# Kernel optimization log

Hardware: AMD Instinct MI355X
Metric: run time of the kernel (lower is better)

The kernel has to match this reference:

```python
import jax, jax.numpy as jnp
import numpy as np

EPS = 0.01       # perturbation radius (constructor arg)
MEAN = 0.1307    # MNIST normalize constants from the 'else' branch
SIGMA = 0.3081


def _get_bound(v, eps):
    # torch get_bound detaches eps before taking |.| and summing
    r = jnp.sum(jnp.abs(jax.lax.stop_gradient(eps)), axis=-1)
    return v + r, v - r


def _relu_zono(v, eps):
    # v: [N], eps: [N, E]. Append one fresh (zero) error column, as the torch code does.
    n = v.shape[0]
    eps = jnp.concatenate([eps, jnp.zeros((n, 1), eps.dtype)], axis=-1)  # [N, E+1]
    u, l = _get_bound(v, eps)
    denom = u - l  # = 2*sum|eps| >= 0; guard against 0 for non-crossing rows
    # slopes are created as Parameters = u/(u-l) on the first pass (detached leaf)
    slope = jax.lax.stop_gradient(u / jnp.where(denom == 0, 1.0, denom))
    # at init slope == base = u/(u-l), so the slope <= base branch is taken
    term = (1.0 - slope) * u * 0.5
    crossing = (u > 0) & (l < 0)
    dead = u <= 0
    # torch uses slope.data * values.data for the linear part, + term (term carries grad)
    v_cross = jax.lax.stop_gradient(slope * v) + term
    v_new = jnp.where(dead, 0.0, jnp.where(crossing, v_cross, v))
    eps_cross = jnp.concatenate([slope[:, None] * eps[:, :-1], term[:, None]], axis=-1)
    eps_new = jnp.where(dead[:, None], 0.0, jnp.where(crossing[:, None], eps_cross, eps))
    return v_new, eps_new


def _forward(inputs, W1, b1, W2, b2, W3, b3):
    # initial zonotope build (faithful to source: values = u + l, radii = values - l = u)
    upper = jnp.minimum(inputs + EPS, 1.0)   # upper - relu(upper - 1)
    lower = jnp.maximum(inputs - EPS, 0.0)   # relu(lower)
    values = upper + lower
    eps = jnp.diag((values - lower).flatten())  # [D, D]
    # Normalize layer (the 'else' branch)
    values = (values - MEAN) / SIGMA
    eps = eps / SIGMA
    # Flatten
    v = values.flatten()
    # Linear -> ReLU -> Linear -> ReLU -> Linear
    v = W1 @ v + b1
    eps = W1 @ eps
    v, eps = _relu_zono(v, eps)
    v = W2 @ v + b2
    eps = W2 @ eps
    v, eps = _relu_zono(v, eps)
    v = W3 @ v + b3
    eps = W3 @ eps
    u, l = _get_bound(v, eps)
    return u, l


def setup_inputs() -> dict:
    key = jax.random.key(0)
    ks = jax.random.split(key, 7)
    D, H, O = 1024, 4096, 10
    inputs = jax.random.uniform(ks[0], (1, 1, 32, 32), jnp.float32)
    W1 = jax.random.normal(ks[1], (H, D), jnp.float32) / np.float32(np.sqrt(D))
    b1 = jax.random.normal(ks[2], (H,), jnp.float32) * 0.01
    W2 = jax.random.normal(ks[3], (H, H), jnp.float32) / np.float32(np.sqrt(H))
    b2 = jax.random.normal(ks[4], (H,), jnp.float32) * 0.01
    W3 = jax.random.normal(ks[5], (O, H), jnp.float32) / np.float32(np.sqrt(H))
    b3 = jax.random.normal(ks[6], (O,), jnp.float32) * 0.01
    return {"inputs": inputs, "W1": W1, "b1": b1, "W2": W2, "b2": b2, "W3": W3, "b3": b3}


def reference(inputs, W1, b1, W2, b2, W3, b3):
    return _forward(inputs, W1, b1, W2, b2, W3, b3)
```

## Files before the change

kernel.cpp:

```cpp
#include <hip/hip_runtime.h>
#include <math.h>

#define ZEPS  0.01f
#define ZMEAN 0.1307f
#define ZSIGMA 0.3081f

constexpr int D = 1024, H = 4096, O = 10;

using short8 = __attribute__((ext_vector_type(8))) short;
using f32x4  = __attribute__((ext_vector_type(4))) float;
typedef unsigned short ushort_t;

__device__ inline unsigned short f2bf(float x) {
    unsigned int u = __float_as_uint(x);
    u += 0x7FFFu + ((u >> 16) & 1u);
    return (unsigned short)(u >> 16);
}
__device__ inline float bf2f(unsigned short h) {
    return __uint_as_float(((unsigned int)h) << 16);
}
__device__ inline unsigned int f2bf2(float a, float b) {
    return (unsigned int)f2bf(a) | ((unsigned int)f2bf(b) << 16);
}

__device__ inline void gl_lds16(const void* g, void* l) {
    __builtin_amdgcn_global_load_lds(
        (const __attribute__((address_space(1))) unsigned int*)g,
        (__attribute__((address_space(3))) unsigned int*)l, 16, 0, 0);
}

__device__ inline float zval(float xv) {
    float up = fminf(xv + ZEPS, 1.f);
    float lo = fmaxf(xv - ZEPS, 0.f);
    return (up + lo - ZMEAN) / ZSIGMA;
}
__device__ inline float zdia(float xv) {
    return fminf(xv + ZEPS, 1.f) / ZSIGMA;
}

__device__ inline void relu_params(float v, float r, float& vout, float& aout, float& tout) {
    float u = v + r, l = v - r;
    float denom = u - l;
    float slope = u / (denom == 0.f ? 1.f : denom);
    float term = (1.f - slope) * u * 0.5f;
    bool dead = (u <= 0.f);
    bool crossing = (u > 0.f) && (l < 0.f);
    vout = dead ? 0.f : (crossing ? (slope * v + term) : v);
    aout = dead ? 0.f : (crossing ? slope : 1.f);
    tout = (!dead && crossing) ? term : 0.f;
}

__global__ __launch_bounds__(256) void k_pre(const float* __restrict__ W1, const float* __restrict__ b1,
                                             const float* __restrict__ x,
                                             float* __restrict__ v1p, float* __restrict__ a1,
                                             float* __restrict__ t1,
                                             const float* __restrict__ W2, ushort_t* __restrict__ W2bf,
                                             float* __restrict__ pbufR) {
    int b = blockIdx.x;
    if (b < 2048) {
        const float* src = W2 + (size_t)b * 8192;
        ushort_t* dst = W2bf + (size_t)b * 8192;
#pragma unroll
        for (int it = 0; it < 4; ++it) {
            int j = it * 2048 + threadIdx.x * 8;
            float4 w0 = *(const float4*)&src[j];
            float4 w1 = *(const float4*)&src[j + 4];
            uint4 o;
            o.x = f2bf2(w0.x, w0.y);
            o.y = f2bf2(w0.z, w0.w);
            o.z = f2bf2(w1.x, w1.y);
            o.w = f2bf2(w1.z, w1.w);
            *(uint4*)&dst[j] = o;
        }
    } else if (b < 3072) {
        int wid = threadIdx.x >> 6, lane = threadIdx.x & 63;
        int i = (b - 2048) * 4 + wid;
        const float* row = W1 + (size_t)i * D;
        float sv = 0.f, sr = 0.f;
#pragma unroll
        for (int it = 0; it < 4; ++it) {
            int j = it * 256 + lane * 4;
            float4 w = *(const float4*)&row[j];
            float4 xx = *(const float4*)&x[j];
            sv += w.x * zval(xx.x) + w.y * zval(xx.y) + w.z * zval(xx.z) + w.w * zval(xx.w);
            sr += fabsf(w.x) * zdia(xx.x) + fabsf(w.y) * zdia(xx.y) +
                  fabsf(w.z) * zdia(xx.z) + fabsf(w.w) * zdia(xx.w);
        }
#pragma unroll
        for (int m = 1; m <= 32; m <<= 1) {
            sv += __shfl_xor(sv, m, 64);
            sr += __shfl_xor(sr, m, 64);
        }
        if (lane == 0) {
            float vo, ao, to;
            relu_params(sv + b1[i], sr, vo, ao, to);
            v1p[i] = vo; a1[i] = ao; t1[i] = to;
        }
    } else {
        for (int k = threadIdx.x; k < O * D; k += 256) pbufR[k] = 0.f;
    }
}

__global__ __launch_bounds__(256) void k_mid(const float* __restrict__ W1, const float* __restrict__ a1,
                                             const float* __restrict__ x, ushort_t* __restrict__ W1sT,
                                             const float* __restrict__ W2, const float* __restrict__ v1p,
                                             const float* __restrict__ t1,
                                             float* __restrict__ v2raw, float* __restrict__ t2raw) {
    int b = blockIdx.x;
    if (b < 1024) {
        int wid = threadIdx.x >> 6, lane = threadIdx.x & 63;
        int i = b * 4 + wid;
        const float* row = W2 + (size_t)i * H;
        float sv = 0.f, st = 0.f;
#pragma unroll 2
        for (int it = 0; it < 8; ++it) {
            int j = it * 512 + lane * 8;
            float4 w0 = *(const float4*)&row[j];
            float4 w1 = *(const float4*)&row[j + 4];
            float4 v0 = *(const float4*)&v1p[j];
            float4 v1 = *(const float4*)&v1p[j + 4];
            float4 t0 = *(const float4*)&t1[j];
            float4 t1v = *(const float4*)&t1[j + 4];
            sv += w0.x * v0.x + w0.y * v0.y + w0.z * v0.z + w0.w * v0.w
                + w1.x * v1.x + w1.y * v1.y + w1.z * v1.z + w1.w * v1.w;
            st += w0.x * t0.x + w0.y * t0.y + w0.z * t0.z + w0.w * t0.w
                + w1.x * t1v.x + w1.y * t1v.y + w1.z * t1v.z + w1.w * t1v.w;
        }
#pragma unroll
        for (int m = 1; m <= 32; m <<= 1) {
            sv += __shfl_xor(sv, m, 64);
            st += __shfl_xor(st, m, 64);
        }
        if (lane == 0) { v2raw[i] = sv; t2raw[i] = st; }
    } else {
        __shared__ float tile[32][33];
        int bb = b - 1024;
        int j0 = (bb & 31) * 32, k0 = (bb >> 5) * 32;
        int r = threadIdx.x >> 3;
        int c = (threadIdx.x & 7) * 4;
        float4 w = *(const float4*)&W1[(size_t)(k0 + r) * D + j0 + c];
        float4 xx = *(const float4*)&x[j0 + c];
        float a = a1[k0 + r];
        tile[r][c + 0] = a * w.x * zdia(xx.x);
        tile[r][c + 1] = a * w.y * zdia(xx.y);
        tile[r][c + 2] = a * w.z * zdia(xx.z);
        tile[r][c + 3] = a * w.w * zdia(xx.w);
        __syncthreads();
        ushort4 o;
        o.x = f2bf(tile[c + 0][r]);
        o.y = f2bf(tile[c + 1][r]);
        o.z = f2bf(tile[c + 2][r]);
        o.w = f2bf(tile[c + 3][r]);
        *(ushort4*)&W1sT[(size_t)(j0 + r) * H + k0 + c] = o;
    }
}

#define GBK 64
__global__ __launch_bounds__(256) void k_gemm_mfma(const ushort_t* __restrict__ A,
                                                   const ushort_t* __restrict__ B,
                                                   ushort_t* __restrict__ C) {
    const int N = D, K = H;
    __shared__ __align__(16) ushort_t As[2][128 * GBK];
    __shared__ __align__(16) ushort_t Bs[2][128 * GBK];
    int orig = blockIdx.x;
    int b = (orig & 7) * 64 + (orig >> 3);
    int z  = b >> 8;
    int xn = (b >> 5) & 7;
    int ym = b & 31;
    int tid = threadIdx.x;
    int wave = tid >> 6, lane = tid & 63;
    int bm = ym * 128, bn = xn * 128;
    int kbeg = z * (K / 2);
    ushort_t* Cz = C + (size_t)z * ((size_t)H * D);
    int wm = (wave >> 1) * 64, wn = (wave & 1) * 64;

    int srow = lane >> 3, scp = (lane & 7) ^ srow;
    int r15 = lane & 15, quad = lane >> 4, key = r15 & 7;

    const int S = (K / 2) / GBK;

    const ushort_t* Ab = A + (size_t)(bm + wave * 32 + srow) * K + kbeg + scp * 8;
    const ushort_t* Bb = B + (size_t)(bn + wave * 32 + srow) * K + kbeg + scp * 8;

    auto issue = [&](int t, int buf) {
#pragma unroll
        for (int g = 0; g < 4; ++g)
            gl_lds16(Ab + (size_t)(g * 8) * K + t * GBK, &As[buf][(wave * 32 + g * 8) * GBK]);
#pragma unroll
        for (int g = 0; g < 4; ++g)
            gl_lds16(Bb + (size_t)(g * 8) * K + t * GBK, &Bs[buf][(wave * 32 + g * 8) * GBK]);
    };

    f32x4 acc[4][4];
#pragma unroll
    for (int p = 0; p < 4; ++p)
#pragma unroll
        for (int q = 0; q < 4; ++q) acc[p][q] = (f32x4){0.f, 0.f, 0.f, 0.f};

    issue(0, 0);
    __syncthreads();

    for (int t = 0; t < S; ++t) {
        int buf = t & 1, nbuf = buf ^ 1;
        if (t + 1 < S) issue(t + 1, nbuf);
#pragma unroll
        for (int kk = 0; kk < 2; ++kk) {
            short8 af[4], bfr[4];
#pragma unroll
            for (int mt = 0; mt < 4; ++mt)
                af[mt] = *(const short8*)&As[buf][(wm + mt * 16 + r15) * GBK + (((kk * 4 + quad) ^ key)) * 8];
#pragma unroll
            for (int nt = 0; nt < 4; ++nt)
                bfr[nt] = *(const short8*)&Bs[buf][(wn + nt * 16 + r15) * GBK + (((kk * 4 + quad) ^ key)) * 8];
#pragma unroll
            for (int mt = 0; mt < 4; ++mt)
#pragma unroll
                for (int nt = 0; nt < 4; ++nt)
                    acc[mt][nt] = __builtin_amdgcn_mfma_f32_16x16x32_bf16(af[mt], bfr[nt], acc[mt][nt], 0, 0, 0);
        }
        __syncthreads();
    }

#pragma unroll
    for (int mt = 0; mt < 4; ++mt) {
        int gr = bm + wm + mt * 16 + quad * 4;
#pragma unroll
        for (int nt = 0; nt < 4; ++nt) {
            int gc = bn + wn + nt * 16 + r15;
            Cz[(size_t)(gr + 0) * N + gc] = f2bf(acc[mt][nt][0]);
            Cz[(size_t)(gr + 1) * N + gc] = f2bf(acc[mt][nt][1]);
            Cz[(size_t)(gr + 2) * N + gc] = f2bf(acc[mt][nt][2]);
            Cz[(size_t)(gr + 3) * N + gc] = f2bf(acc[mt][nt][3]);
        }
    }
}

__global__ __launch_bounds__(256) void k_relu2(const ushort_t* __restrict__ e1, const ushort_t* __restrict__ e2,
                                               const float* __restrict__ v2raw, const float* __restrict__ t2raw,
                                               const float* __restrict__ b2, const float* __restrict__ W3,
                                               float* __restrict__ v2p, float* __restrict__ a2,
                                               float* __restrict__ t2, float* __restrict__ t2col,
                                               float* __restrict__ w3s) {
    int wid = threadIdx.x >> 6, lane = threadIdx.x & 63;
    int i = blockIdx.x * 4 + wid;
    float s = 0.f;
#pragma unroll
    for (int it = 0; it < 2; ++it) {
        int j = lane * 8 + it * 512;
        ushort4 a0 = *(const ushort4*)&e1[(size_t)i * D + j];
        ushort4 a1v = *(const ushort4*)&e1[(size_t)i * D + j + 4];
        ushort4 b0 = *(const ushort4*)&e2[(size_t)i * D + j];
        ushort4 b1v = *(const ushort4*)&e2[(size_t)i * D + j + 4];
        s += fabsf(bf2f(a0.x) + bf2f(b0.x)) + fabsf(bf2f(a0.y) + bf2f(b0.y))
           + fabsf(bf2f(a0.z) + bf2f(b0.z)) + fabsf(bf2f(a0.w) + bf2f(b0.w))
           + fabsf(bf2f(a1v.x) + bf2f(b1v.x)) + fabsf(bf2f(a1v.y) + bf2f(b1v.y))
           + fabsf(bf2f(a1v.z) + bf2f(b1v.z)) + fabsf(bf2f(a1v.w) + bf2f(b1v.w));
    }
#pragma unroll
    for (int m = 1; m <= 32; m <<= 1) s += __shfl_xor(s, m, 64);
    float ve = v2raw[i];
    float te = t2raw[i];
    float vo, ao, to;
    relu_params(ve + b2[i], s + fabsf(te), vo, ao, to);
    if (lane == 0) { v2p[i] = vo; a2[i] = ao; t2[i] = to; t2col[i] = te; }
    if (lane < O) w3s[(size_t)i * O + lane] = W3[(size_t)lane * H + i] * ao;
}

__global__ __launch_bounds__(256) void k_eps3a(const ushort_t* __restrict__ e1, const ushort_t* __restrict__ e2,
                                               const float* __restrict__ w3s,
                                               float* __restrict__ pbufR) {
    int jb = blockIdx.x, ib = blockIdx.y;
    int jj = threadIdx.x & 15, s = threadIdx.x >> 4;
    int j = jb * 64 + jj * 4;
    int i0 = ib * 128 + s * 8;
    float acc[4][O];
#pragma unroll
    for (int c = 0; c < 4; ++c)
#pragma unroll
        for (int o = 0; o < O; ++o) acc[c][o] = 0.f;
    for (int ii = 0; ii < 8; ++ii) {
        int i = i0 + ii;
        ushort4 a = *(const ushort4*)&e1[(size_t)i * D + j];
        ushort4 b = *(const ushort4*)&e2[(size_t)i * D + j];
        float e0 = bf2f(a.x) + bf2f(b.x), ee1 = bf2f(a.y) + bf2f(b.y);
        float ee2 = bf2f(a.z) + bf2f(b.z), ee3 = bf2f(a.w) + bf2f(b.w);
        const float* w = &w3s[(size_t)i * O];
#pragma unroll
        for (int o = 0; o < O; ++o) {
            float wo = w[o];
            acc[0][o] += wo * e0; acc[1][o] += wo * ee1;
            acc[2][o] += wo * ee2; acc[3][o] += wo * ee3;
        }
    }
    __shared__ float sm[16][64][O];
#pragma unroll
    for (int c = 0; c < 4; ++c)
#pragma unroll
        for (int o = 0; o < O; ++o) sm[s][jj * 4 + c][o] = acc[c][o];
    __syncthreads();
    for (int idx = threadIdx.x; idx < 64 * O; idx += 256) {
        int col = idx / O, o = idx % O;
        float t = 0.f;
#pragma unroll
        for (int ss = 0; ss < 16; ++ss) t += sm[ss][col][o];
        atomicAdd(&pbufR[(size_t)o * D + jb * 64 + col], t);
    }
}

__global__ __launch_bounds__(256) void k_final(const float* __restrict__ W3, const float* __restrict__ b3,
                                               const float* __restrict__ v2p, const float* __restrict__ a2,
                                               const float* __restrict__ t2col, const float* __restrict__ t2,
                                               const float* __restrict__ pbufR, float* __restrict__ out) {
    int o = blockIdx.x, tid = threadIdx.x;
    float s3 = 0.f;
    for (int j = tid; j < D; j += 256) s3 += fabsf(pbufR[(size_t)o * D + j]);
    const float* row = W3 + (size_t)o * H;
    float sv = 0.f, s1 = 0.f, s2 = 0.f;
    for (int i = tid; i < H; i += 256) {
        float w = row[i];
        sv += w * v2p[i];
        s1 += w * a2[i] * t2col[i];
        s2 += w * t2[i];
    }
    __shared__ float ra[256], rb[256], rc[256], rd[256];
    ra[tid] = sv; rb[tid] = s1; rc[tid] = s2; rd[tid] = s3;
    __syncthreads();
    for (int off = 128; off; off >>= 1) {
        if (tid < off) {
            ra[tid] += ra[tid + off]; rb[tid] += rb[tid + off];
            rc[tid] += rc[tid + off]; rd[tid] += rd[tid + off];
        }
        __syncthreads();
    }
    if (tid == 0) {
        float v3 = ra[0] + b3[o];
        float rr = rd[0] + fabsf(rb[0]) + fabsf(rc[0]);
        out[o] = v3 + rr;
        out[O + o] = v3 - rr;
    }
}

extern "C" void kernel_launch(void* const* d_in, const int* in_sizes, int n_in,
                              void* d_out, int out_size, void* d_ws, size_t ws_size,
                              hipStream_t stream) {
    const float* x  = (const float*)d_in[0];
    const float* W1 = (const float*)d_in[1];
    const float* b1 = (const float*)d_in[2];
    const float* W2 = (const float*)d_in[3];
    const float* b2 = (const float*)d_in[4];
    const float* W3 = (const float*)d_in[5];
    const float* b3 = (const float*)d_in[6];
    float* out = (float*)d_out;

    float* p = (float*)d_ws;
    float* v1p    = p; p += H;
    float* a1     = p; p += H;
    float* t1     = p; p += H;
    float* t2col  = p; p += H;
    float* v2p    = p; p += H;
    float* a2     = p; p += H;
    float* t2     = p; p += H;
    float* v2raw  = p; p += H;
    float* t2raw  = p; p += H;
    float* w3s    = p; p += H * O + 8;
    float* pbufR  = p; p += O * D + 8;
    ushort_t* eps2  = (ushort_t*)p;
    ushort_t* W1sT  = eps2 + (size_t)2 * H * D;
    ushort_t* W2bf  = W1sT + (size_t)H * D;
    ushort_t* eps2b = eps2 + (size_t)H * D;

    k_pre<<<3073, 256, 0, stream>>>(W1, b1, x, v1p, a1, t1, W2, W2bf, pbufR);
    k_mid<<<5120, 256, 0, stream>>>(W1, a1, x, W1sT, W2, v1p, t1, v2raw, t2raw);
    k_gemm_mfma<<<512, 256, 0, stream>>>(W2bf, W1sT, eps2);
    k_relu2<<<H / 4, 256, 0, stream>>>(eps2, eps2b, v2raw, t2raw, b2, W3, v2p, a2, t2, t2col, w3s);
    k_eps3a<<<dim3(D / 64, 32), 256, 0, stream>>>(eps2, eps2b, w3s, pbufR);
    k_final<<<O, 256, 0, stream>>>(W3, b3, v2p, a2, t2col, t2, pbufR, out);
}
```

Before: 223.5 us.

## Fuse W2 bf16 conversion into matvec, drop split-K GEMM, fold relu2 into epilogue

The W2 fp32-to-bf16 conversion moves into the k_mid matvec so W2 is read from memory once instead of twice. The GEMM stops splitting K into two halves and uses 128x64 tiles over the full K, so only one bf16 eps matrix is written and no second partial has to be summed. The GEMM epilogue accumulates per-row |eps| sums into r2acc with atomics, which removes the separate k_relu2 pass over eps. The relu parameters are recomputed inside k_eps3a and k_final. The trade-off is a longer K loop per block with a smaller N tile, plus atomic traffic in the epilogue.

```diff
diff --git a/kernel.cpp b/kernel.cpp
--- a/kernel.cpp
+++ b/kernel.cpp
@@ -54,27 +54,11 @@
                                              const float* __restrict__ x,
                                              float* __restrict__ v1p, float* __restrict__ a1,
                                              float* __restrict__ t1,
-                                             const float* __restrict__ W2, ushort_t* __restrict__ W2bf,
-                                             float* __restrict__ pbufR) {
+                                             float* __restrict__ r2acc, float* __restrict__ pbufR) {
     int b = blockIdx.x;
-    if (b < 2048) {
-        const float* src = W2 + (size_t)b * 8192;
-        ushort_t* dst = W2bf + (size_t)b * 8192;
-#pragma unroll
-        for (int it = 0; it < 4; ++it) {
-            int j = it * 2048 + threadIdx.x * 8;
-            float4 w0 = *(const float4*)&src[j];
-            float4 w1 = *(const float4*)&src[j + 4];
-            uint4 o;
-            o.x = f2bf2(w0.x, w0.y);
-            o.y = f2bf2(w0.z, w0.w);
-            o.z = f2bf2(w1.x, w1.y);
-            o.w = f2bf2(w1.z, w1.w);
-            *(uint4*)&dst[j] = o;
-        }
-    } else if (b < 3072) {
+    if (b < 1024) {
         int wid = threadIdx.x >> 6, lane = threadIdx.x & 63;
-        int i = (b - 2048) * 4 + wid;
+        int i = b * 4 + wid;
         const float* row = W1 + (size_t)i * D;
         float sv = 0.f, sr = 0.f;
 #pragma unroll
@@ -97,6 +81,7 @@
             v1p[i] = vo; a1[i] = ao; t1[i] = to;
         }
     } else {
+        for (int k = threadIdx.x; k < H; k += 256) r2acc[k] = 0.f;
         for (int k = threadIdx.x; k < O * D; k += 256) pbufR[k] = 0.f;
     }
 }
@@ -104,13 +89,14 @@
 __global__ __launch_bounds__(256) void k_mid(const float* __restrict__ W1, const float* __restrict__ a1,
                                              const float* __restrict__ x, ushort_t* __restrict__ W1sT,
                                              const float* __restrict__ W2, const float* __restrict__ v1p,
-                                             const float* __restrict__ t1,
+                                             const float* __restrict__ t1, ushort_t* __restrict__ W2bf,
                                              float* __restrict__ v2raw, float* __restrict__ t2raw) {
     int b = blockIdx.x;
     if (b < 1024) {
         int wid = threadIdx.x >> 6, lane = threadIdx.x & 63;
         int i = b * 4 + wid;
         const float* row = W2 + (size_t)i * H;
+        ushort_t* orow = W2bf + (size_t)i * H;
         float sv = 0.f, st = 0.f;
 #pragma unroll 2
         for (int it = 0; it < 8; ++it) {
@@ -125,6 +111,12 @@
                 + w1.x * v1.x + w1.y * v1.y + w1.z * v1.z + w1.w * v1.w;
             st += w0.x * t0.x + w0.y * t0.y + w0.z * t0.z + w0.w * t0.w
                 + w1.x * t1v.x + w1.y * t1v.y + w1.z * t1v.z + w1.w * t1v.w;
+            uint4 o;
+            o.x = f2bf2(w0.x, w0.y);
+            o.y = f2bf2(w0.z, w0.w);
+            o.z = f2bf2(w1.x, w1.y);
+            o.w = f2bf2(w1.z, w1.w);
+            *(uint4*)&orow[j] = o;
         }
 #pragma unroll
         for (int m = 1; m <= 32; m <<= 1) {
@@ -158,44 +150,42 @@
 #define GBK 64
 __global__ __launch_bounds__(256) void k_gemm_mfma(const ushort_t* __restrict__ A,
                                                    const ushort_t* __restrict__ B,
-                                                   ushort_t* __restrict__ C) {
+                                                   ushort_t* __restrict__ C,
+                                                   float* __restrict__ r2acc) {
     const int N = D, K = H;
     __shared__ __align__(16) ushort_t As[2][128 * GBK];
-    __shared__ __align__(16) ushort_t Bs[2][128 * GBK];
+    __shared__ __align__(16) ushort_t Bs[2][64 * GBK];
     int orig = blockIdx.x;
     int b = (orig & 7) * 64 + (orig >> 3);
-    int z  = b >> 8;
-    int xn = (b >> 5) & 7;
-    int ym = b & 31;
+    int ym = b >> 4;
+    int xn = b & 15;
     int tid = threadIdx.x;
     int wave = tid >> 6, lane = tid & 63;
-    int bm = ym * 128, bn = xn * 128;
-    int kbeg = z * (K / 2);
-    ushort_t* Cz = C + (size_t)z * ((size_t)H * D);
-    int wm = (wave >> 1) * 64, wn = (wave & 1) * 64;
+    int bm = ym * 128, bn = xn * 64;
+    int wm = (wave >> 1) * 64, wn = (wave & 1) * 32;
 
     int srow = lane >> 3, scp = (lane & 7) ^ srow;
     int r15 = lane & 15, quad = lane >> 4, key = r15 & 7;
 
-    const int S = (K / 2) / GBK;
-
-    const ushort_t* Ab = A + (size_t)(bm + wave * 32 + srow) * K + kbeg + scp * 8;
-    const ushort_t* Bb = B + (size_t)(bn + wave * 32 + srow) * K + kbeg + scp * 8;
+    const int S = K / GBK;
+
+    const ushort_t* Ab = A + (size_t)(bm + wave * 32 + srow) * K + scp * 8;
+    const ushort_t* Bb = B + (size_t)(bn + wave * 16 + srow) * K + scp * 8;
 
     auto issue = [&](int t, int buf) {
 #pragma unroll
         for (int g = 0; g < 4; ++g)
             gl_lds16(Ab + (size_t)(g * 8) * K + t * GBK, &As[buf][(wave * 32 + g * 8) * GBK]);
 #pragma unroll
-        for (int g = 0; g < 4; ++g)
-            gl_lds16(Bb + (size_t)(g * 8) * K + t * GBK, &Bs[buf][(wave * 32 + g * 8) * GBK]);
+        for (int g = 0; g < 2; ++g)
+            gl_lds16(Bb + (size_t)(g * 8) * K + t * GBK, &Bs[buf][(wave * 16 + g * 8) * GBK]);
     };
 
-    f32x4 acc[4][4];
+    f32x4 acc[4][2];
 #pragma unroll
     for (int p = 0; p < 4; ++p)
 #pragma unroll
-        for (int q = 0; q < 4; ++q) acc[p][q] = (f32x4){0.f, 0.f, 0.f, 0.f};
+        for (int q = 0; q < 2; ++q) acc[p][q] = (f32x4){0.f, 0.f, 0.f, 0.f};
 
     issue(0, 0);
     __syncthreads();
@@ -205,74 +195,79 @@
         if (t + 1 < S) issue(t + 1, nbuf);
 #pragma unroll
         for (int kk = 0; kk < 2; ++kk) {
-            short8 af[4], bfr[4];
+            short8 af[4], bfr[2];
 #pragma unroll
             for (int mt = 0; mt < 4; ++mt)
                 af[mt] = *(const short8*)&As[buf][(wm + mt * 16 + r15) * GBK + (((kk * 4 + quad) ^ key)) * 8];
 #pragma unroll
-            for (int nt = 0; nt < 4; ++nt)
+            for (int nt = 0; nt < 2; ++nt)
                 bfr[nt] = *(const short8*)&Bs[buf][(wn + nt * 16 + r15) * GBK + (((kk * 4 + quad) ^ key)) * 8];
 #pragma unroll
             for (int mt = 0; mt < 4; ++mt)
 #pragma unroll
-                for (int nt = 0; nt < 4; ++nt)
+                for (int nt = 0; nt < 2; ++nt)
                     acc[mt][nt] = __builtin_amdgcn_mfma_f32_16x16x32_bf16(af[mt], bfr[nt], acc[mt][nt], 0, 0, 0);
         }
         __syncthreads();
     }
 
+    float rsum[4][4];
+#pragma unroll
+    for (int mt = 0; mt < 4; ++mt)
+#pragma unroll
+        for (int rg = 0; rg < 4; ++rg) rsum[mt][rg] = 0.f;
 #pragma unroll
     for (int mt = 0; mt < 4; ++mt) {
         int gr = bm + wm + mt * 16 + quad * 4;
 #pragma unroll
-        for (int nt = 0; nt < 4; ++nt) {
+        for (int nt = 0; nt < 2; ++nt) {
             int gc = bn + wn + nt * 16 + r15;
-            Cz[(size_t)(gr + 0) * N + gc] = f2bf(acc[mt][nt][0]);
-            Cz[(size_t)(gr + 1) * N + gc] = f2bf(acc[mt][nt][1]);
-            Cz[(size_t)(gr + 2) * N + gc] = f2bf(acc[mt][nt][2]);
-            Cz[(size_t)(gr + 3) * N + gc] = f2bf(acc[mt][nt][3]);
-        }
-    }
-}
-
-__global__ __launch_bounds__(256) void k_relu2(const ushort_t* __restrict__ e1, const ushort_t* __restrict__ e2,
-                                               const float* __restrict__ v2raw, const float* __restrict__ t2raw,
-                                               const float* __restrict__ b2, const float* __restrict__ W3,
-                                               float* __restrict__ v2p, float* __restrict__ a2,
-                                               float* __restrict__ t2, float* __restrict__ t2col,
-                                               float* __restrict__ w3s) {
-    int wid = threadIdx.x >> 6, lane = threadIdx.x & 63;
-    int i = blockIdx.x * 4 + wid;
-    float s = 0.f;
-#pragma unroll
-    for (int it = 0; it < 2; ++it) {
-        int j = lane * 8 + it * 512;
-        ushort4 a0 = *(const ushort4*)&e1[(size_t)i * D + j];
-        ushort4 a1v = *(const ushort4*)&e1[(size_t)i * D + j + 4];
-        ushort4 b0 = *(const ushort4*)&e2[(size_t)i * D + j];
-        ushort4 b1v = *(const ushort4*)&e2[(size_t)i * D + j + 4];
-        s += fabsf(bf2f(a0.x) + bf2f(b0.x)) + fabsf(bf2f(a0.y) + bf2f(b0.y))
-           + fabsf(bf2f(a0.z) + bf2f(b0.z)) + fabsf(bf2f(a0.w) + bf2f(b0.w))
-           + fabsf(bf2f(a1v.x) + bf2f(b1v.x)) + fabsf(bf2f(a1v.y) + bf2f(b1v.y))
-           + fabsf(bf2f(a1v.z) + bf2f(b1v.z)) + fabsf(bf2f(a1v.w) + bf2f(b1v.w));
-    }
-#pragma unroll
-    for (int m = 1; m <= 32; m <<= 1) s += __shfl_xor(s, m, 64);
-    float ve = v2raw[i];
-    float te = t2raw[i];
-    float vo, ao, to;
-    relu_params(ve + b2[i], s + fabsf(te), vo, ao, to);
-    if (lane == 0) { v2p[i] = vo; a2[i] = ao; t2[i] = to; t2col[i] = te; }
-    if (lane < O) w3s[(size_t)i * O + lane] = W3[(size_t)lane * H + i] * ao;
-}
-
-__global__ __launch_bounds__(256) void k_eps3a(const ushort_t* __restrict__ e1, const ushort_t* __restrict__ e2,
-                                               const float* __restrict__ w3s,
+            f32x4 a = acc[mt][nt];
+#pragma unroll
+            for (int rg = 0; rg < 4; ++rg) {
+                ushort_t hb = f2bf(a[rg]);
+                C[(size_t)(gr + rg) * N + gc] = hb;
+                rsum[mt][rg] += fabsf(bf2f(hb));
+            }
+        }
+    }
+#pragma unroll
+    for (int mt = 0; mt < 4; ++mt)
+#pragma unroll
+        for (int rg = 0; rg < 4; ++rg) {
+            float v = rsum[mt][rg];
+            v += __shfl_xor(v, 1, 64);
+            v += __shfl_xor(v, 2, 64);
+            v += __shfl_xor(v, 4, 64);
+            v += __shfl_xor(v, 8, 64);
+            if (r15 == 0)
+                atomicAdd(&r2acc[bm + wm + mt * 16 + quad * 4 + rg], v);
+        }
+}
+
+__global__ __launch_bounds__(256) void k_eps3a(const ushort_t* __restrict__ e,
+                                               const float* __restrict__ r2acc,
+                                               const float* __restrict__ v2raw,
+                                               const float* __restrict__ t2raw,
+                                               const float* __restrict__ b2,
+                                               const float* __restrict__ W3,
                                                float* __restrict__ pbufR) {
     int jb = blockIdx.x, ib = blockIdx.y;
+    __shared__ float w3sm[128][O];
+    int i0b = ib * 128;
+    if (threadIdx.x < 128) {
+        int i = i0b + threadIdx.x;
+        float te = t2raw[i];
+        float vo, ao, to;
+        relu_params(v2raw[i] + b2[i], r2acc[i] + fabsf(te), vo, ao, to);
+#pragma unroll
+        for (int o = 0; o < O; ++o) w3sm[threadIdx.x][o] = W3[(size_t)o * H + i] * ao;
+    }
+    __syncthreads();
+
     int jj = threadIdx.x & 15, s = threadIdx.x >> 4;
     int j = jb * 64 + jj * 4;
-    int i0 = ib * 128 + s * 8;
+    int i0 = i0b + s * 8;
     float acc[4][O];
 #pragma unroll
     for (int c = 0; c < 4; ++c)
@@ -280,11 +275,10 @@
         for (int o = 0; o < O; ++o) acc[c][o] = 0.f;
     for (int ii = 0; ii < 8; ++ii) {
         int i = i0 + ii;
-        ushort4 a = *(const ushort4*)&e1[(size_t)i * D + j];
-        ushort4 b = *(const ushort4*)&e2[(size_t)i * D + j];
-        float e0 = bf2f(a.x) + bf2f(b.x), ee1 = bf2f(a.y) + bf2f(b.y);
-        float ee2 = bf2f(a.z) + bf2f(b.z), ee3 = bf2f(a.w) + bf2f(b.w);
-        const float* w = &w3s[(size_t)i * O];
+        ushort4 a = *(const ushort4*)&e[(size_t)i * D + j];
+        float e0 = bf2f(a.x), ee1 = bf2f(a.y);
+        float ee2 = bf2f(a.z), ee3 = bf2f(a.w);
+        const float* w = &w3sm[i - i0b][0];
 #pragma unroll
         for (int o = 0; o < O; ++o) {
             float wo = w[o];
@@ -308,8 +302,10 @@
 }
 
 __global__ __launch_bounds__(256) void k_final(const float* __restrict__ W3, const float* __restrict__ b3,
-                                               const float* __restrict__ v2p, const float* __restrict__ a2,
-                                               const float* __restrict__ t2col, const float* __restrict__ t2,
+                                               const float* __restrict__ r2acc,
+                                               const float* __restrict__ v2raw,
+                                               const float* __restrict__ t2raw,
+                                               const float* __restrict__ b2,
                                                const float* __restrict__ pbufR, float* __restrict__ out) {
     int o = blockIdx.x, tid = threadIdx.x;
     float s3 = 0.f;
@@ -318,9 +314,12 @@
     float sv = 0.f, s1 = 0.f, s2 = 0.f;
     for (int i = tid; i < H; i += 256) {
         float w = row[i];
-        sv += w * v2p[i];
-        s1 += w * a2[i] * t2col[i];
-        s2 += w * t2[i];
+        float te = t2raw[i];
+        float vo, ao, to;
+        relu_params(v2raw[i] + b2[i], r2acc[i] + fabsf(te), vo, ao, to);
+        sv += w * vo;
+        s1 += w * ao * te;
+        s2 += w * to;
     }
     __shared__ float ra[256], rb[256], rc[256], rd[256];
     ra[tid] = sv; rb[tid] = s1; rc[tid] = s2; rd[tid] = s3;
@@ -356,23 +355,17 @@
     float* v1p    = p; p += H;
     float* a1     = p; p += H;
     float* t1     = p; p += H;
-    float* t2col  = p; p += H;
-    float* v2p    = p; p += H;
-    float* a2     = p; p += H;
-    float* t2     = p; p += H;
     float* v2raw  = p; p += H;
     float* t2raw  = p; p += H;
-    float* w3s    = p; p += H * O + 8;
+    float* r2acc  = p; p += H;
     float* pbufR  = p; p += O * D + 8;
-    ushort_t* eps2  = (ushort_t*)p;
-    ushort_t* W1sT  = eps2 + (size_t)2 * H * D;
+    ushort_t* eps   = (ushort_t*)p;
+    ushort_t* W1sT  = eps + (size_t)H * D;
     ushort_t* W2bf  = W1sT + (size_t)H * D;
-    ushort_t* eps2b = eps2 + (size_t)H * D;
-
-    k_pre<<<3073, 256, 0, stream>>>(W1, b1, x, v1p, a1, t1, W2, W2bf, pbufR);
-    k_mid<<<5120, 256, 0, stream>>>(W1, a1, x, W1sT, W2, v1p, t1, v2raw, t2raw);
-    k_gemm_mfma<<<512, 256, 0, stream>>>(W2bf, W1sT, eps2);
-    k_relu2<<<H / 4, 256, 0, stream>>>(eps2, eps2b, v2raw, t2raw, b2, W3, v2p, a2, t2, t2col, w3s);
-    k_eps3a<<<dim3(D / 64, 32), 256, 0, stream>>>(eps2, eps2b, w3s, pbufR);
-    k_final<<<O, 256, 0, stream>>>(W3, b3, v2p, a2, t2col, t2, pbufR, out);
-}
+
+    k_pre<<<1025, 256, 0, stream>>>(W1, b1, x, v1p, a1, t1, r2acc, pbufR);
+    k_mid<<<5120, 256, 0, stream>>>(W1, a1, x, W1sT, W2, v1p, t1, W2bf, v2raw, t2raw);
+    k_gemm_mfma<<<512, 256, 0, stream>>>(W2bf, W1sT, eps, r2acc);
+    k_eps3a<<<dim3(D / 64, 32), 256, 0, stream>>>(eps, r2acc, v2raw, t2raw, b2, W3, pbufR);
+    k_final<<<O, 256, 0, stream>>>(W3, b3, r2acc, v2raw, t2raw, b2, pbufR, out);
+}
```

Result: slower. 245.3 us (+9.8%).

## Fuse W2 bf16 conversion into matvec and merge relu2 with eps3 reduction

Applied to the files above, without the earlier changes.

The W2 fp32-to-bf16 conversion moves from k_pre into the k_mid matvec loop, so W2 is read from global memory once instead of twice. k_relu2 and k_eps3a are merged into one k_epsfuse kernel: each block computes the ReLU parameters for 16 rows, keeps the scaled W3 slice in LDS, and accumulates those rows' eps contributions. The atomic accumulation now targets 32 partitioned partial buffers, and k_final sums them. The GEMM block-index mapping also changes from the swizzled order to a plain one, which may alter L2 locality. The trade-offs are more atomics per thread and only 256 blocks in the fused kernel.

```diff
diff --git a/kernel.cpp b/kernel.cpp
--- a/kernel.cpp
+++ b/kernel.cpp
@@ -8,6 +8,7 @@
 constexpr int D = 1024, H = 4096, O = 10;
 
 using short8 = __attribute__((ext_vector_type(8))) short;
+using us8    = __attribute__((ext_vector_type(8))) unsigned short;
 using f32x4  = __attribute__((ext_vector_type(4))) float;
 typedef unsigned short ushort_t;
 
@@ -54,27 +55,11 @@
                                              const float* __restrict__ x,
                                              float* __restrict__ v1p, float* __restrict__ a1,
                                              float* __restrict__ t1,
-                                             const float* __restrict__ W2, ushort_t* __restrict__ W2bf,
-                                             float* __restrict__ pbufR) {
+                                             float* __restrict__ pbufP) {
     int b = blockIdx.x;
-    if (b < 2048) {
-        const float* src = W2 + (size_t)b * 8192;
-        ushort_t* dst = W2bf + (size_t)b * 8192;
-#pragma unroll
-        for (int it = 0; it < 4; ++it) {
-            int j = it * 2048 + threadIdx.x * 8;
-            float4 w0 = *(const float4*)&src[j];
-            float4 w1 = *(const float4*)&src[j + 4];
-            uint4 o;
-            o.x = f2bf2(w0.x, w0.y);
-            o.y = f2bf2(w0.z, w0.w);
-            o.z = f2bf2(w1.x, w1.y);
-            o.w = f2bf2(w1.z, w1.w);
-            *(uint4*)&dst[j] = o;
-        }
-    } else if (b < 3072) {
+    if (b < 1024) {
         int wid = threadIdx.x >> 6, lane = threadIdx.x & 63;
-        int i = (b - 2048) * 4 + wid;
+        int i = b * 4 + wid;
         const float* row = W1 + (size_t)i * D;
         float sv = 0.f, sr = 0.f;
 #pragma unroll
@@ -97,20 +82,23 @@
             v1p[i] = vo; a1[i] = ao; t1[i] = to;
         }
     } else {
-        for (int k = threadIdx.x; k < O * D; k += 256) pbufR[k] = 0.f;
+        int zb = b - 1024;
+        size_t base = (size_t)zb * 5120;
+        for (int k = threadIdx.x; k < 5120; k += 256) pbufP[base + k] = 0.f;
     }
 }
 
 __global__ __launch_bounds__(256) void k_mid(const float* __restrict__ W1, const float* __restrict__ a1,
                                              const float* __restrict__ x, ushort_t* __restrict__ W1sT,
                                              const float* __restrict__ W2, const float* __restrict__ v1p,
-                                             const float* __restrict__ t1,
+                                             const float* __restrict__ t1, ushort_t* __restrict__ W2bf,
                                              float* __restrict__ v2raw, float* __restrict__ t2raw) {
     int b = blockIdx.x;
     if (b < 1024) {
         int wid = threadIdx.x >> 6, lane = threadIdx.x & 63;
         int i = b * 4 + wid;
         const float* row = W2 + (size_t)i * H;
+        ushort_t* orow = W2bf + (size_t)i * H;
         float sv = 0.f, st = 0.f;
 #pragma unroll 2
         for (int it = 0; it < 8; ++it) {
@@ -125,6 +113,12 @@
                 + w1.x * v1.x + w1.y * v1.y + w1.z * v1.z + w1.w * v1.w;
             st += w0.x * t0.x + w0.y * t0.y + w0.z * t0.z + w0.w * t0.w
                 + w1.x * t1v.x + w1.y * t1v.y + w1.z * t1v.z + w1.w * t1v.w;
+            uint4 o;
+            o.x = f2bf2(w0.x, w0.y);
+            o.y = f2bf2(w0.z, w0.w);
+            o.z = f2bf2(w1.x, w1.y);
+            o.w = f2bf2(w1.z, w1.w);
+            *(uint4*)&orow[j] = o;
         }
 #pragma unroll
         for (int m = 1; m <= 32; m <<= 1) {
@@ -162,33 +156,32 @@
     const int N = D, K = H;
     __shared__ __align__(16) ushort_t As[2][128 * GBK];
     __shared__ __align__(16) ushort_t Bs[2][128 * GBK];
-    int orig = blockIdx.x;
-    int b = (orig & 7) * 64 + (orig >> 3);
-    int z  = b >> 8;
-    int xn = (b >> 5) & 7;
-    int ym = b & 31;
+    int b = blockIdx.x;
+    int xb = b & 7;
+    int v = b >> 3;
+    int z = v & 1;
+    int y = v >> 1;
     int tid = threadIdx.x;
     int wave = tid >> 6, lane = tid & 63;
-    int bm = ym * 128, bn = xn * 128;
+    int bm = y * 128, bn = xb * 128;
     int kbeg = z * (K / 2);
     ushort_t* Cz = C + (size_t)z * ((size_t)H * D);
     int wm = (wave >> 1) * 64, wn = (wave & 1) * 64;
 
-    int srow = lane >> 3, scp = (lane & 7) ^ srow;
+    int srow = lane >> 3, sc = lane & 7, scp = sc ^ srow;
     int r15 = lane & 15, quad = lane >> 4, key = r15 & 7;
 
     const int S = (K / 2) / GBK;
 
-    const ushort_t* Ab = A + (size_t)(bm + wave * 32 + srow) * K + kbeg + scp * 8;
-    const ushort_t* Bb = B + (size_t)(bn + wave * 32 + srow) * K + kbeg + scp * 8;
-
-    auto issue = [&](int t, int buf) {
-#pragma unroll
-        for (int g = 0; g < 4; ++g)
-            gl_lds16(Ab + (size_t)(g * 8) * K + t * GBK, &As[buf][(wave * 32 + g * 8) * GBK]);
-#pragma unroll
-        for (int g = 0; g < 4; ++g)
-            gl_lds16(Bb + (size_t)(g * 8) * K + t * GBK, &Bs[buf][(wave * 32 + g * 8) * GBK]);
+    auto issue = [&](int s, int buf) {
+#pragma unroll
+        for (int g = 0; g < 4; ++g) {
+            int row = wave * 32 + g * 8;
+            gl_lds16(&A[(size_t)(bm + row + srow) * K + kbeg + s * GBK + scp * 8],
+                     &As[buf][row * GBK]);
+            gl_lds16(&B[(size_t)(bn + row + srow) * K + kbeg + s * GBK + scp * 8],
+                     &Bs[buf][row * GBK]);
+        }
     };
 
     f32x4 acc[4][4];
@@ -200,9 +193,9 @@
     issue(0, 0);
     __syncthreads();
 
-    for (int t = 0; t < S; ++t) {
-        int buf = t & 1, nbuf = buf ^ 1;
-        if (t + 1 < S) issue(t + 1, nbuf);
+    for (int s = 0; s < S; ++s) {
+        int buf = s & 1, nbuf = buf ^ 1;
+        if (s + 1 < S) issue(s + 1, nbuf);
 #pragma unroll
         for (int kk = 0; kk < 2; ++kk) {
             short8 af[4], bfr[4];
@@ -235,91 +228,87 @@
     }
 }
 
-__global__ __launch_bounds__(256) void k_relu2(const ushort_t* __restrict__ e1, const ushort_t* __restrict__ e2,
-                                               const float* __restrict__ v2raw, const float* __restrict__ t2raw,
-                                               const float* __restrict__ b2, const float* __restrict__ W3,
-                                               float* __restrict__ v2p, float* __restrict__ a2,
-                                               float* __restrict__ t2, float* __restrict__ t2col,
-                                               float* __restrict__ w3s) {
-    int wid = threadIdx.x >> 6, lane = threadIdx.x & 63;
-    int i = blockIdx.x * 4 + wid;
-    float s = 0.f;
-#pragma unroll
-    for (int it = 0; it < 2; ++it) {
-        int j = lane * 8 + it * 512;
-        ushort4 a0 = *(const ushort4*)&e1[(size_t)i * D + j];
-        ushort4 a1v = *(const ushort4*)&e1[(size_t)i * D + j + 4];
-        ushort4 b0 = *(const ushort4*)&e2[(size_t)i * D + j];
-        ushort4 b1v = *(const ushort4*)&e2[(size_t)i * D + j + 4];
-        s += fabsf(bf2f(a0.x) + bf2f(b0.x)) + fabsf(bf2f(a0.y) + bf2f(b0.y))
-           + fabsf(bf2f(a0.z) + bf2f(b0.z)) + fabsf(bf2f(a0.w) + bf2f(b0.w))
-           + fabsf(bf2f(a1v.x) + bf2f(b1v.x)) + fabsf(bf2f(a1v.y) + bf2f(b1v.y))
-           + fabsf(bf2f(a1v.z) + bf2f(b1v.z)) + fabsf(bf2f(a1v.w) + bf2f(b1v.w));
-    }
-#pragma unroll
-    for (int m = 1; m <= 32; m <<= 1) s += __shfl_xor(s, m, 64);
-    float ve = v2raw[i];
-    float te = t2raw[i];
-    float vo, ao, to;
-    relu_params(ve + b2[i], s + fabsf(te), vo, ao, to);
-    if (lane == 0) { v2p[i] = vo; a2[i] = ao; t2[i] = to; t2col[i] = te; }
-    if (lane < O) w3s[(size_t)i * O + lane] = W3[(size_t)lane * H + i] * ao;
-}
-
-__global__ __launch_bounds__(256) void k_eps3a(const ushort_t* __restrict__ e1, const ushort_t* __restrict__ e2,
-                                               const float* __restrict__ w3s,
-                                               float* __restrict__ pbufR) {
-    int jb = blockIdx.x, ib = blockIdx.y;
-    int jj = threadIdx.x & 15, s = threadIdx.x >> 4;
-    int j = jb * 64 + jj * 4;
-    int i0 = ib * 128 + s * 8;
+__global__ __launch_bounds__(256) void k_epsfuse(const ushort_t* __restrict__ e1, const ushort_t* __restrict__ e2,
+                                                 const float* __restrict__ v2raw, const float* __restrict__ t2raw,
+                                                 const float* __restrict__ b2, const float* __restrict__ W3,
+                                                 float* __restrict__ v2p, float* __restrict__ a2,
+                                                 float* __restrict__ t2, float* __restrict__ pbufP) {
+    __shared__ float w3sm[16][O];
+    int b = blockIdx.x, tid = threadIdx.x;
+    int wid = tid >> 6, lane = tid & 63;
+    int i0 = b * 16;
+
+#pragma unroll
+    for (int rr = 0; rr < 4; ++rr) {
+        int il = wid * 4 + rr;
+        int i = i0 + il;
+        const ushort_t* p1 = &e1[(size_t)i * D + lane * 16];
+        const ushort_t* p2 = &e2[(size_t)i * D + lane * 16];
+        float s = 0.f;
+#pragma unroll
+        for (int q = 0; q < 2; ++q) {
+            us8 u1 = *(const us8*)(p1 + q * 8);
+            us8 u2 = *(const us8*)(p2 + q * 8);
+#pragma unroll
+            for (int e = 0; e < 8; ++e) s += fabsf(bf2f(u1[e]) + bf2f(u2[e]));
+        }
+#pragma unroll
+        for (int m = 1; m <= 32; m <<= 1) s += __shfl_xor(s, m, 64);
+        float te = t2raw[i];
+        float vo, ao, to;
+        relu_params(v2raw[i] + b2[i], s + fabsf(te), vo, ao, to);
+        if (lane == 0) { v2p[i] = vo; a2[i] = ao; t2[i] = to; }
+        if (lane < O) w3sm[il][lane] = W3[(size_t)lane * H + i] * ao;
+    }
+    __syncthreads();
+
+    int j = tid * 4;
     float acc[4][O];
 #pragma unroll
     for (int c = 0; c < 4; ++c)
 #pragma unroll
         for (int o = 0; o < O; ++o) acc[c][o] = 0.f;
-    for (int ii = 0; ii < 8; ++ii) {
-        int i = i0 + ii;
+#pragma unroll 4
+    for (int il = 0; il < 16; ++il) {
+        int i = i0 + il;
         ushort4 a = *(const ushort4*)&e1[(size_t)i * D + j];
-        ushort4 b = *(const ushort4*)&e2[(size_t)i * D + j];
-        float e0 = bf2f(a.x) + bf2f(b.x), ee1 = bf2f(a.y) + bf2f(b.y);
-        float ee2 = bf2f(a.z) + bf2f(b.z), ee3 = bf2f(a.w) + bf2f(b.w);
-        const float* w = &w3s[(size_t)i * O];
+        ushort4 bb = *(const ushort4*)&e2[(size_t)i * D + j];
+        float es0 = bf2f(a.x) + bf2f(bb.x), es1 = bf2f(a.y) + bf2f(bb.y);
+        float es2 = bf2f(a.z) + bf2f(bb.z), es3 = bf2f(a.w) + bf2f(bb.w);
+        const float* w = &w3sm[il][0];
 #pragma unroll
         for (int o = 0; o < O; ++o) {
             float wo = w[o];
-            acc[0][o] += wo * e0; acc[1][o] += wo * ee1;
-            acc[2][o] += wo * ee2; acc[3][o] += wo * ee3;
-        }
-    }
-    __shared__ float sm[16][64][O];
-#pragma unroll
-    for (int c = 0; c < 4; ++c)
-#pragma unroll
-        for (int o = 0; o < O; ++o) sm[s][jj * 4 + c][o] = acc[c][o];
-    __syncthreads();
-    for (int idx = threadIdx.x; idx < 64 * O; idx += 256) {
-        int col = idx / O, o = idx % O;
-        float t = 0.f;
-#pragma unroll
-        for (int ss = 0; ss < 16; ++ss) t += sm[ss][col][o];
-        atomicAdd(&pbufR[(size_t)o * D + jb * 64 + col], t);
-    }
+            acc[0][o] += wo * es0; acc[1][o] += wo * es1;
+            acc[2][o] += wo * es2; acc[3][o] += wo * es3;
+        }
+    }
+    float* pg = &pbufP[(size_t)(b & 31) * O * D];
+#pragma unroll
+    for (int o = 0; o < O; ++o)
+#pragma unroll
+        for (int c = 0; c < 4; ++c)
+            atomicAdd(&pg[(size_t)o * D + j + c], acc[c][o]);
 }
 
 __global__ __launch_bounds__(256) void k_final(const float* __restrict__ W3, const float* __restrict__ b3,
                                                const float* __restrict__ v2p, const float* __restrict__ a2,
-                                               const float* __restrict__ t2col, const float* __restrict__ t2,
-                                               const float* __restrict__ pbufR, float* __restrict__ out) {
+                                               const float* __restrict__ t2, const float* __restrict__ t2raw,
+                                               const float* __restrict__ pbufP, float* __restrict__ out) {
     int o = blockIdx.x, tid = threadIdx.x;
     float s3 = 0.f;
-    for (int j = tid; j < D; j += 256) s3 += fabsf(pbufR[(size_t)o * D + j]);
+    for (int j = tid; j < D; j += 256) {
+        float t = 0.f;
+#pragma unroll
+        for (int g = 0; g < 32; ++g) t += pbufP[((size_t)g * O + o) * D + j];
+        s3 += fabsf(t);
+    }
     const float* row = W3 + (size_t)o * H;
     float sv = 0.f, s1 = 0.f, s2 = 0.f;
     for (int i = tid; i < H; i += 256) {
         float w = row[i];
         sv += w * v2p[i];
-        s1 += w * a2[i] * t2col[i];
+        s1 += w * a2[i] * t2raw[i];
         s2 += w * t2[i];
     }
     __shared__ float ra[256], rb[256], rc[256], rd[256];
@@ -356,23 +345,20 @@
     float* v1p    = p; p += H;
     float* a1     = p; p += H;
     float* t1     = p; p += H;
-    float* t2col  = p; p += H;
+    float* v2raw  = p; p += H;
+    float* t2raw  = p; p += H;
     float* v2p    = p; p += H;
     float* a2     = p; p += H;
     float* t2     = p; p += H;
-    float* v2raw  = p; p += H;
-    float* t2raw  = p; p += H;
-    float* w3s    = p; p += H * O + 8;
-    float* pbufR  = p; p += O * D + 8;
+    float* pbufP  = p; p += 32 * O * D + 8;
     ushort_t* eps2  = (ushort_t*)p;
     ushort_t* W1sT  = eps2 + (size_t)2 * H * D;
     ushort_t* W2bf  = W1sT + (size_t)H * D;
     ushort_t* eps2b = eps2 + (size_t)H * D;
 
-    k_pre<<<3073, 256, 0, stream>>>(W1, b1, x, v1p, a1, t1, W2, W2bf, pbufR);
-    k_mid<<<5120, 256, 0, stream>>>(W1, a1, x, W1sT, W2, v1p, t1, v2raw, t2raw);
+    k_pre<<<1088, 256, 0, stream>>>(W1, b1, x, v1p, a1, t1, pbufP);
+    k_mid<<<5120, 256, 0, stream>>>(W1, a1, x, W1sT, W2, v1p, t1, W2bf, v2raw, t2raw);
     k_gemm_mfma<<<512, 256, 0, stream>>>(W2bf, W1sT, eps2);
-    k_relu2<<<H / 4, 256, 0, stream>>>(eps2, eps2b, v2raw, t2raw, b2, W3, v2p, a2, t2, t2col, w3s);
-    k_eps3a<<<dim3(D / 64, 32), 256, 0, stream>>>(eps2, eps2b, w3s, pbufR);
-    k_final<<<O, 256, 0, stream>>>(W3, b3, v2p, a2, t2col, t2, pbufR, out);
-}
+    k_epsfuse<<<256, 256, 0, stream>>>(eps2, eps2b, v2raw, t2raw, b2, W3, v2p, a2, t2, pbufP);
+    k_final<<<O, 256, 0, stream>>>(W3, b3, v2p, a2, t2, t2raw, pbufP, out);
+}
```

New measurement: 242.6 us. +8.6%, slower.
